# Kernel optimization log

Measured on AMD Instinct MI355X. Metric: run time of the kernel, lower is better.

## Reference

```python
import jax, jax.numpy as jnp
import numpy as np

BN_EPS = 1e-3  # keras BatchNormalization default epsilon


def setup_inputs() -> dict:
    key = jax.random.key(0)
    ks = jax.random.split(key, 7)
    B, W, D, H, C = 2, 32, 32, 32, 256
    x = jax.random.normal(ks[0], (B, W, D, H, C), dtype=jnp.float32)
    # Stacked params for the 4 branches: [query, key, judge, value]
    conv_w = jax.random.normal(ks[1], (4, C, C), dtype=jnp.float32) / np.sqrt(C).astype(np.float32)
    conv_b = jax.random.normal(ks[2], (4, C), dtype=jnp.float32) * 0.01
    bn_scale = 1.0 + 0.1 * jax.random.normal(ks[3], (4, C), dtype=jnp.float32)
    bn_offset = 0.1 * jax.random.normal(ks[4], (4, C), dtype=jnp.float32)
    bn_mean = 0.1 * jax.random.normal(ks[5], (4, C), dtype=jnp.float32)
    bn_var = jax.random.uniform(ks[6], (4, C), dtype=jnp.float32, minval=0.5, maxval=1.5)
    gamma = jnp.asarray(1e-4, dtype=jnp.float32)  # scalar residual scale (init 0.0001 in source)
    return dict(x=x, conv_w=conv_w, conv_b=conv_b, bn_scale=bn_scale,
                bn_offset=bn_offset, bn_mean=bn_mean, bn_var=bn_var, gamma=gamma)


def _branch(x, w, b, s, o, m, v):
    # Conv3D 1x1x1 == per-voxel channel mixing, then inference-mode BN, then ReLU
    y = jnp.einsum('bwdhc,cf->bwdhf', x, w) + b
    y = s * (y - m) * jax.lax.rsqrt(v + BN_EPS) + o
    return jax.nn.relu(y)


def reference(x, conv_w, conv_b, bn_scale, bn_offset, bn_mean, bn_var, gamma):
    B, W, D, H, C = x.shape
    N = W * D * H
    # Raw reshape (B,W,D,H,C) -> (B,C,N), matching keras Reshape((C,-1)) on channels-last layout
    def br(i):
        return _branch(x, conv_w[i], conv_b[i], bn_scale[i], bn_offset[i],
                       bn_mean[i], bn_var[i]).reshape(B, C, N)
    Q, K, J, V = br(0), br(1), br(2), br(3)
    m1 = jnp.matmul(K, jnp.swapaxes(Q, 1, 2))   # (B, C, C)
    m2 = jnp.matmul(K, jnp.swapaxes(J, 1, 2))   # (B, C, C)
    affinity = jax.nn.sigmoid(jnp.matmul(m1, m2))  # (B, C, C), sigmoid not softmax
    weights = jnp.matmul(affinity, V)           # (B, C, N)
    weights = weights.reshape(B, W, D, H, C)    # raw reshape back, as in source
    return gamma * weights + x
```

## Files before the change

kernel.cpp:

```cpp
#include <hip/hip_runtime.h>
#include <math.h>

typedef __attribute__((ext_vector_type(4))) float  f32x4;
typedef __attribute__((ext_vector_type(8))) short  s16x8;
typedef __attribute__((ext_vector_type(4))) short  s16x4;

#define BN_EPS 1e-3f

static constexpr int    CC    = 256;
static constexpr int    NVOX  = 32768;
static constexpr int    BATCH = 2;
static constexpr int    MTOT  = BATCH * NVOX;
static constexpr size_t ELEM_BR = (size_t)MTOT * CC;
static constexpr size_t SZ_BR   = ELEM_BR * 2;
static constexpr size_t WS_Q   = 0;
static constexpr size_t WS_K   = WS_Q  + SZ_BR;
static constexpr size_t WS_J   = WS_K  + SZ_BR;
static constexpr size_t WS_V   = WS_J  + SZ_BR;
static constexpr size_t WS_M1  = WS_V  + SZ_BR;
static constexpr size_t WS_M2  = WS_M1 + (size_t)BATCH*CC*CC*4;
static constexpr size_t WS_AFF = WS_M2 + (size_t)BATCH*CC*CC*4;
static constexpr size_t WS_WT  = WS_AFF + (size_t)BATCH*CC*CC*2;
static constexpr size_t WS_AB  = WS_WT + (size_t)4*CC*CC*2;

__device__ __forceinline__ short f2bf(float f) {
  union { float f; unsigned u; } v; v.f = f;
  unsigned u = v.u + 0x7FFFu + ((v.u >> 16) & 1u);
  return (short)(u >> 16);
}

__global__ __launch_bounds__(256) void k0_prep(
    const float* __restrict__ conv_w, const float* __restrict__ conv_b,
    const float* __restrict__ bn_s, const float* __restrict__ bn_o,
    const float* __restrict__ bn_m, const float* __restrict__ bn_v,
    char* __restrict__ ws)
{
  int t = blockIdx.x * 256 + threadIdx.x;
  ((float*)(ws + WS_M1))[t] = 0.f;
  int f = t >> 16, rem = t & 65535;
  int cin = rem >> 8, cout = rem & 255;
  ((short*)(ws + WS_WT))[f*65536 + cout*256 + cin] = f2bf(conv_w[t]);
  if (t < 1024) {
    float alpha = bn_s[t] * rsqrtf(bn_v[t] + BN_EPS);
    float beta  = alpha * (conv_b[t] - bn_m[t]) + bn_o[t];
    float* ab = (float*)(ws + WS_AB);
    ab[t] = alpha; ab[1024 + t] = beta;
  }
}

__global__ __launch_bounds__(256, 2) void k1_branches(
    const float* __restrict__ x, char* __restrict__ ws)
{
  __shared__ short As[64 * 256];
  __shared__ short Bs[64 * 256];
  __shared__ short Rs[64][72];

  const int tid = threadIdx.x;
  const int m0  = blockIdx.x * 64;
  const int lane = tid & 63, wid = tid >> 6;
  const int wm = wid >> 1, wn = wid & 1;
  const int lr = lane & 15, lg = lane >> 4;

  const short* Wt = (const short*)(ws + WS_WT);
  const float* ab = (const float*)(ws + WS_AB);

  #pragma unroll
  for (int it = 0; it < 16; ++it) {
    int idx = tid + 256 * it;
    int r = idx >> 6, c4 = (idx & 63) << 2;
    const float4 v = *(const float4*)(x + (size_t)(m0 + r) * 256 + c4);
    s16x4 s; s[0]=f2bf(v.x); s[1]=f2bf(v.y); s[2]=f2bf(v.z); s[3]=f2bf(v.w);
    int u = c4 >> 3;
    int swz = (((u & 24) | ((u ^ r) & 7)) << 3) | (c4 & 7);
    *(s16x4*)&As[r * 256 + swz] = s;
  }

  {
    const short* Wf = Wt;
    #pragma unroll
    for (int i = 0; i < 8; ++i) {
      int slot = i * 256 + tid;
      int cout = slot >> 5, u = slot & 31;
      int usrc = (u & 24) | ((u ^ cout) & 7);
      const short* src = Wf + cout * 256 + usrc * 8;
      short* dst = Bs + (size_t)(i * 256 + wid * 64) * 8;
      __builtin_amdgcn_global_load_lds(
          (const __attribute__((address_space(1))) void*)src,
          (__attribute__((address_space(3))) void*)dst, 16, 0, 0);
    }
  }

  __syncthreads();

  for (int nt = 0; nt < 16; ++nt) {
    const int f  = nt >> 2;
    const int c0 = (nt & 3) * 64;

    f32x4 acc[2][2];
    #pragma unroll
    for (int a = 0; a < 2; ++a)
      #pragma unroll
      for (int b = 0; b < 2; ++b) { f32x4 z = {0.f,0.f,0.f,0.f}; acc[a][b] = z; }

    #pragma unroll
    for (int k0 = 0; k0 < 8; ++k0) {
      const int ua = k0 * 4 + lg;
      s16x8 af[2], bf[2];
      #pragma unroll
      for (int mi = 0; mi < 2; ++mi) {
        int r = wm*32 + mi*16 + lr;
        int uu = (ua & 24) | ((ua ^ r) & 7);
        af[mi] = *(const s16x8*)&As[r * 256 + uu * 8];
      }
      #pragma unroll
      for (int nj = 0; nj < 2; ++nj) {
        int c = wn*32 + nj*16 + lr;
        int uu = (ua & 24) | ((ua ^ c) & 7);
        bf[nj] = *(const s16x8*)&Bs[c * 256 + uu * 8];
      }
      #pragma unroll
      for (int mi = 0; mi < 2; ++mi)
        #pragma unroll
        for (int nj = 0; nj < 2; ++nj)
          acc[mi][nj] = __builtin_amdgcn_mfma_f32_16x16x32_bf16(
              bf[nj], af[mi], acc[mi][nj], 0, 0, 0);
    }

    __syncthreads();

    if (nt < 15) {
      const int fn  = (nt + 1) >> 2;
      const int c0n = ((nt + 1) & 3) * 64;
      const short* Wf = Wt + fn * 65536 + c0n * 256;
      #pragma unroll
      for (int i = 0; i < 8; ++i) {
        int slot = i * 256 + tid;
        int cout = slot >> 5, u = slot & 31;
        int usrc = (u & 24) | ((u ^ cout) & 7);
        const short* src = Wf + cout * 256 + usrc * 8;
        short* dst = Bs + (size_t)(i * 256 + wid * 64) * 8;
        __builtin_amdgcn_global_load_lds(
            (const __attribute__((address_space(1))) void*)src,
            (__attribute__((address_space(3))) void*)dst, 16, 0, 0);
      }
    }

    #pragma unroll
    for (int nj = 0; nj < 2; ++nj) {
      int c4b = c0 + wn*32 + nj*16 + lg*4;
      const f32x4 al = *(const f32x4*)&ab[f*256 + c4b];
      const f32x4 be = *(const f32x4*)&ab[1024 + f*256 + c4b];
      #pragma unroll
      for (int mi = 0; mi < 2; ++mi) {
        s16x4 s;
        #pragma unroll
        for (int ii = 0; ii < 4; ++ii) {
          float yv = al[ii] * acc[mi][nj][ii] + be[ii];
          yv = yv > 0.f ? yv : 0.f;
          s[ii] = f2bf(yv);
        }
        *(s16x4*)&Rs[wm*32 + mi*16 + lr][wn*32 + nj*16 + lg*4] = s;
      }
    }

    __syncthreads();

    short* Yf = (short*)(ws + (size_t)f * SZ_BR);
    #pragma unroll
    for (int it = 0; it < 2; ++it) {
      int idx = tid + 256 * it;
      int r = idx >> 3, c8 = (idx & 7) << 3;
      *(s16x8*)&Yf[(size_t)(m0 + r) * 256 + c0 + c8] = *(const s16x8*)&Rs[r][c8];
    }
  }
}

__global__ __launch_bounds__(256, 2) void k2_m1m2(char* __restrict__ ws)
{
  __shared__ short Ks[128][88], Qs[128][88], Js[128][88];

  const int tid = threadIdx.x;
  const int chunk = blockIdx.x;
  const int ti = blockIdx.y >> 1, tj = blockIdx.y & 1;
  const int b  = blockIdx.z;
  const size_t boff = (size_t)b * NVOX * CC;
  const short* Qm = (const short*)(ws + WS_Q) + boff;
  const short* Km = (const short*)(ws + WS_K) + boff;
  const short* Jm = (const short*)(ws + WS_J) + boff;

  const int lane = tid & 63, wid = tid >> 6;
  const int wm = wid >> 1, wn = wid & 1;
  const int lr = lane & 15, lg = lane >> 4;

  f32x4 accq[4][4], accj[4][4];
  #pragma unroll
  for (int a = 0; a < 4; ++a)
    #pragma unroll
    for (int c = 0; c < 4; ++c) { f32x4 z = {0.f,0.f,0.f,0.f}; accq[a][c] = z; accj[a][c] = z; }

  const int nstart = chunk * 1024;
  for (int n0 = nstart; n0 < nstart + 1024; n0 += 64) {
    __syncthreads();
    #pragma unroll
    for (int it = 0; it < 4; ++it) {
      int idx = tid + 256 * it;
      int r = idx >> 3, n8 = (idx & 7) << 3;
      *(s16x8*)&Ks[r][n8] = *(const s16x8*)&Km[(size_t)(ti*128 + r)*NVOX + n0 + n8];
      *(s16x8*)&Qs[r][n8] = *(const s16x8*)&Qm[(size_t)(tj*128 + r)*NVOX + n0 + n8];
      *(s16x8*)&Js[r][n8] = *(const s16x8*)&Jm[(size_t)(tj*128 + r)*NVOX + n0 + n8];
    }
    __syncthreads();
    #pragma unroll
    for (int ks = 0; ks < 2; ++ks) {
      s16x8 a[4], bq[4], bj[4];
      #pragma unroll
      for (int mi = 0; mi < 4; ++mi)
        a[mi] = *(const s16x8*)&Ks[wm*64 + mi*16 + lr][ks*32 + lg*8];
      #pragma unroll
      for (int nj = 0; nj < 4; ++nj) {
        bq[nj] = *(const s16x8*)&Qs[wn*64 + nj*16 + lr][ks*32 + lg*8];
        bj[nj] = *(const s16x8*)&Js[wn*64 + nj*16 + lr][ks*32 + lg*8];
      }
      #pragma unroll
      for (int mi = 0; mi < 4; ++mi)
        #pragma unroll
        for (int nj = 0; nj < 4; ++nj) {
          accq[mi][nj] = __builtin_amdgcn_mfma_f32_16x16x32_bf16(a[mi], bq[nj], accq[mi][nj], 0,0,0);
          accj[mi][nj] = __builtin_amdgcn_mfma_f32_16x16x32_bf16(a[mi], bj[nj], accj[mi][nj], 0,0,0);
        }
    }
  }
  float* m1 = (float*)(ws + WS_M1) + (size_t)b * CC * CC;
  float* m2 = (float*)(ws + WS_M2) + (size_t)b * CC * CC;
  #pragma unroll
  for (int mi = 0; mi < 4; ++mi)
    #pragma unroll
    for (int nj = 0; nj < 4; ++nj)
      #pragma unroll
      for (int ii = 0; ii < 4; ++ii) {
        int i = ti*128 + wm*64 + mi*16 + lg*4 + ii;
        int j = tj*128 + wn*64 + nj*16 + lr;
        atomicAdd(&m1[i*256 + j], accq[mi][nj][ii]);
        atomicAdd(&m2[i*256 + j], accj[mi][nj][ii]);
      }
}

__global__ __launch_bounds__(256) void k3_aff(char* __restrict__ ws)
{
  const int j = threadIdx.x;
  const int i = blockIdx.x & 255;
  const int b = blockIdx.x >> 8;
  const float* m1 = (const float*)(ws + WS_M1) + (size_t)b * CC * CC;
  const float* m2 = (const float*)(ws + WS_M2) + (size_t)b * CC * CC;
  float z = 0.f;
  #pragma unroll 8
  for (int k = 0; k < 256; ++k)
    z = fmaf(m1[i*256 + k], m2[k*256 + j], z);
  float a = 1.f / (1.f + expf(-z));
  ((short*)(ws + WS_AFF))[(size_t)b*CC*CC + i*256 + j] = f2bf(a);
}

__global__ __launch_bounds__(256, 2) void k4_out(
    const float* __restrict__ x, const float* __restrict__ gamma_p,
    char* __restrict__ ws, float* __restrict__ out)
{
  __shared__ short As[128][88];
  __shared__ short Vs[128][88];

  const int tid = threadIdx.x;
  const int n0 = blockIdx.x * 128;
  const int i0 = blockIdx.y * 128;
  const int b  = blockIdx.z;
  const float gamma = gamma_p[0];
  const short* aff = (const short*)(ws + WS_AFF) + (size_t)b * CC * CC;
  const short* Vm  = (const short*)(ws + WS_V) + (size_t)b * NVOX * CC;

  const int lane = tid & 63, wid = tid >> 6;
  const int wm = wid >> 1, wn = wid & 1;
  const int lr = lane & 15, lg = lane >> 4;

  f32x4 acc[4][4];
  #pragma unroll
  for (int a = 0; a < 4; ++a)
    #pragma unroll
    for (int c = 0; c < 4; ++c) { f32x4 z = {0.f,0.f,0.f,0.f}; acc[a][c] = z; }

  for (int c0 = 0; c0 < 256; c0 += 64) {
    __syncthreads();
    #pragma unroll
    for (int it = 0; it < 4; ++it) {
      int idx = tid + 256 * it;
      int r = idx >> 3, c8 = (idx & 7) << 3;
      *(s16x8*)&As[r][c8] = *(const s16x8*)&aff[(size_t)(i0 + r)*256 + c0 + c8];
    }
    #pragma unroll
    for (int it = 0; it < 4; ++it) {
      int idx = tid + 256 * it;
      int t15 = idx & 15;
      int cc = idx >> 4, n8 = t15 << 3;
      s16x8 v = *(const s16x8*)&Vm[(size_t)(c0 + cc)*NVOX + n0 + n8];
      #pragma unroll
      for (int uu = 0; uu < 8; ++uu) {
        int u = (uu + t15) & 7;
        Vs[n8 + u][cc] = v[u];
      }
    }
    __syncthreads();
    #pragma unroll
    for (int ks = 0; ks < 2; ++ks) {
      s16x8 a[4], bv[4];
      #pragma unroll
      for (int mi = 0; mi < 4; ++mi)
        a[mi] = *(const s16x8*)&As[wm*64 + mi*16 + lr][ks*32 + lg*8];
      #pragma unroll
      for (int nj = 0; nj < 4; ++nj)
        bv[nj] = *(const s16x8*)&Vs[wn*64 + nj*16 + lr][ks*32 + lg*8];
      #pragma unroll
      for (int mi = 0; mi < 4; ++mi)
        #pragma unroll
        for (int nj = 0; nj < 4; ++nj)
          acc[mi][nj] = __builtin_amdgcn_mfma_f32_16x16x32_bf16(a[mi], bv[nj], acc[mi][nj], 0,0,0);
    }
  }
  #pragma unroll
  for (int mi = 0; mi < 4; ++mi)
    #pragma unroll
    for (int nj = 0; nj < 4; ++nj)
      #pragma unroll
      for (int ii = 0; ii < 4; ++ii) {
        int i = i0 + wm*64 + mi*16 + lg*4 + ii;
        int n = n0 + wn*64 + nj*16 + lr;
        size_t flat = (size_t)b * NVOX * CC + (size_t)i * NVOX + n;
        out[flat] = gamma * acc[mi][nj][ii] + x[flat];
      }
}

extern "C" void kernel_launch(void* const* d_in, const int* in_sizes, int n_in,
                              void* d_out, int out_size, void* d_ws, size_t ws_size,
                              hipStream_t stream)
{
  const float* x      = (const float*)d_in[0];
  const float* conv_w = (const float*)d_in[1];
  const float* conv_b = (const float*)d_in[2];
  const float* bn_s   = (const float*)d_in[3];
  const float* bn_o   = (const float*)d_in[4];
  const float* bn_m   = (const float*)d_in[5];
  const float* bn_v   = (const float*)d_in[6];
  const float* gamma  = (const float*)d_in[7];
  char*  ws  = (char*)d_ws;
  float* out = (float*)d_out;

  k0_prep    <<<1024, 256, 0, stream>>>(conv_w, conv_b, bn_s, bn_o, bn_m, bn_v, ws);
  k1_branches<<<1024, 256, 0, stream>>>(x, ws);
  k2_m1m2    <<<dim3(32, 4, 2), 256, 0, stream>>>(ws);
  k3_aff     <<<512, 256, 0, stream>>>(ws);
  k4_out     <<<dim3(256, 2, 2), 256, 0, stream>>>(x, gamma, ws, out);
}
```

Before: 188.4 us.

## Widen output kernel to full 256-row tiles and vectorize epilogue stores

The final affinity×V kernel now uses 512-thread blocks that each cover all 256 affinity rows for a 128-voxel slice. Each V tile is loaded once instead of twice, and the grid halves. The MFMA operands are swapped so each lane holds four consecutive voxels, which allows float4 loads of x and float4 stores of out in place of scalar accesses. The LDS swizzle in the branch kernel is also changed to XOR the high chunk bits with the row, aiming to reduce bank conflicts. In exchange, LDS use per block rises and fewer blocks may fit on each CU.

Result: faster. 182.7 us (-3.0%).

```diff
diff --git a/kernel.cpp b/kernel.cpp
--- a/kernel.cpp
+++ b/kernel.cpp
@@ -71,7 +71,7 @@
     const float4 v = *(const float4*)(x + (size_t)(m0 + r) * 256 + c4);
     s16x4 s; s[0]=f2bf(v.x); s[1]=f2bf(v.y); s[2]=f2bf(v.z); s[3]=f2bf(v.w);
     int u = c4 >> 3;
-    int swz = (((u & 24) | ((u ^ r) & 7)) << 3) | (c4 & 7);
+    int swz = ((u ^ ((r & 7) << 2)) << 3) | (c4 & 7);
     *(s16x4*)&As[r * 256 + swz] = s;
   }
 
@@ -81,7 +81,7 @@
     for (int i = 0; i < 8; ++i) {
       int slot = i * 256 + tid;
       int cout = slot >> 5, u = slot & 31;
-      int usrc = (u & 24) | ((u ^ cout) & 7);
+      int usrc = u ^ ((cout & 7) << 2);
       const short* src = Wf + cout * 256 + usrc * 8;
       short* dst = Bs + (size_t)(i * 256 + wid * 64) * 8;
       __builtin_amdgcn_global_load_lds(
@@ -109,13 +109,13 @@
       #pragma unroll
       for (int mi = 0; mi < 2; ++mi) {
         int r = wm*32 + mi*16 + lr;
-        int uu = (ua & 24) | ((ua ^ r) & 7);
+        int uu = ua ^ ((r & 7) << 2);
         af[mi] = *(const s16x8*)&As[r * 256 + uu * 8];
       }
       #pragma unroll
       for (int nj = 0; nj < 2; ++nj) {
         int c = wn*32 + nj*16 + lr;
-        int uu = (ua & 24) | ((ua ^ c) & 7);
+        int uu = ua ^ ((c & 7) << 2);
         bf[nj] = *(const s16x8*)&Bs[c * 256 + uu * 8];
       }
       #pragma unroll
@@ -136,7 +136,7 @@
       for (int i = 0; i < 8; ++i) {
         int slot = i * 256 + tid;
         int cout = slot >> 5, u = slot & 31;
-        int usrc = (u & 24) | ((u ^ cout) & 7);
+        int usrc = u ^ ((cout & 7) << 2);
         const short* src = Wf + cout * 256 + usrc * 8;
         short* dst = Bs + (size_t)(i * 256 + wid * 64) * 8;
         __builtin_amdgcn_global_load_lds(
@@ -260,23 +260,22 @@
   ((short*)(ws + WS_AFF))[(size_t)b*CC*CC + i*256 + j] = f2bf(a);
 }
 
-__global__ __launch_bounds__(256, 2) void k4_out(
+__global__ __launch_bounds__(512, 4) void k4_out(
     const float* __restrict__ x, const float* __restrict__ gamma_p,
     char* __restrict__ ws, float* __restrict__ out)
 {
-  __shared__ short As[128][88];
-  __shared__ short Vs[128][88];
+  __shared__ short affS[256][72];
+  __shared__ short Vs[128][72];
 
   const int tid = threadIdx.x;
   const int n0 = blockIdx.x * 128;
-  const int i0 = blockIdx.y * 128;
-  const int b  = blockIdx.z;
+  const int b  = blockIdx.y;
   const float gamma = gamma_p[0];
   const short* aff = (const short*)(ws + WS_AFF) + (size_t)b * CC * CC;
   const short* Vm  = (const short*)(ws + WS_V) + (size_t)b * NVOX * CC;
 
   const int lane = tid & 63, wid = tid >> 6;
-  const int wm = wid >> 1, wn = wid & 1;
+  const int wi = wid >> 1, wn = wid & 1;
   const int lr = lane & 15, lg = lane >> 4;
 
   f32x4 acc[4][4];
@@ -289,16 +288,16 @@
     __syncthreads();
     #pragma unroll
     for (int it = 0; it < 4; ++it) {
-      int idx = tid + 256 * it;
+      int idx = tid + 512 * it;
       int r = idx >> 3, c8 = (idx & 7) << 3;
-      *(s16x8*)&As[r][c8] = *(const s16x8*)&aff[(size_t)(i0 + r)*256 + c0 + c8];
-    }
-    #pragma unroll
-    for (int it = 0; it < 4; ++it) {
-      int idx = tid + 256 * it;
+      *(s16x8*)&affS[r][c8] = *(const s16x8*)&aff[(size_t)r * 256 + c0 + c8];
+    }
+    #pragma unroll
+    for (int it = 0; it < 2; ++it) {
+      int idx = tid + 512 * it;
       int t15 = idx & 15;
       int cc = idx >> 4, n8 = t15 << 3;
-      s16x8 v = *(const s16x8*)&Vm[(size_t)(c0 + cc)*NVOX + n0 + n8];
+      s16x8 v = *(const s16x8*)&Vm[(size_t)(c0 + cc) * NVOX + n0 + n8];
       #pragma unroll
       for (int uu = 0; uu < 8; ++uu) {
         int u = (uu + t15) & 7;
@@ -308,10 +307,10 @@
     __syncthreads();
     #pragma unroll
     for (int ks = 0; ks < 2; ++ks) {
-      s16x8 a[4], bv[4];
+      s16x8 af[4], bv[4];
       #pragma unroll
       for (int mi = 0; mi < 4; ++mi)
-        a[mi] = *(const s16x8*)&As[wm*64 + mi*16 + lr][ks*32 + lg*8];
+        af[mi] = *(const s16x8*)&affS[wi*64 + mi*16 + lr][ks*32 + lg*8];
       #pragma unroll
       for (int nj = 0; nj < 4; ++nj)
         bv[nj] = *(const s16x8*)&Vs[wn*64 + nj*16 + lr][ks*32 + lg*8];
@@ -319,20 +318,25 @@
       for (int mi = 0; mi < 4; ++mi)
         #pragma unroll
         for (int nj = 0; nj < 4; ++nj)
-          acc[mi][nj] = __builtin_amdgcn_mfma_f32_16x16x32_bf16(a[mi], bv[nj], acc[mi][nj], 0,0,0);
+          acc[mi][nj] = __builtin_amdgcn_mfma_f32_16x16x32_bf16(
+              bv[nj], af[mi], acc[mi][nj], 0, 0, 0);
     }
   }
   #pragma unroll
   for (int mi = 0; mi < 4; ++mi)
     #pragma unroll
-    for (int nj = 0; nj < 4; ++nj)
-      #pragma unroll
-      for (int ii = 0; ii < 4; ++ii) {
-        int i = i0 + wm*64 + mi*16 + lg*4 + ii;
-        int n = n0 + wn*64 + nj*16 + lr;
-        size_t flat = (size_t)b * NVOX * CC + (size_t)i * NVOX + n;
-        out[flat] = gamma * acc[mi][nj][ii] + x[flat];
-      }
+    for (int nj = 0; nj < 4; ++nj) {
+      int i = wi*64 + mi*16 + lr;
+      int n = n0 + wn*64 + nj*16 + lg*4;
+      size_t flat = (size_t)b * NVOX * CC + (size_t)i * NVOX + n;
+      const float4 xv = *(const float4*)(x + flat);
+      float4 o;
+      o.x = gamma * acc[mi][nj][0] + xv.x;
+      o.y = gamma * acc[mi][nj][1] + xv.y;
+      o.z = gamma * acc[mi][nj][2] + xv.z;
+      o.w = gamma * acc[mi][nj][3] + xv.w;
+      *(float4*)(out + flat) = o;
+    }
 }
 
 extern "C" void kernel_launch(void* const* d_in, const int* in_sizes, int n_in,
@@ -354,5 +358,5 @@
   k1_branches<<<1024, 256, 0, stream>>>(x, ws);
   k2_m1m2    <<<dim3(32, 4, 2), 256, 0, stream>>>(ws);
   k3_aff     <<<512, 256, 0, stream>>>(ws);
-  k4_out     <<<dim3(256, 2, 2), 256, 0, stream>>>(x, gamma, ws, out);
-}
+  k4_out     <<<dim3(256, 2), 512, 0, stream>>>(x, gamma, ws, out);
+}
```
